# Kernel tuning notes

Measured on AMD Instinct MI355X. Metric: run time of the kernel, lower is better.

## Reference

```python
import jax, jax.numpy as jnp
import numpy as np

N, E = 50000, 800000
H_IN, H, L = 256, 128, 3
EPS = 1e-5  # BatchNorm1d default eps


def setup_inputs() -> dict:
    key = jax.random.key(0)
    ks = jax.random.split(key, 8)
    x = jax.random.normal(ks[0], (N, H_IN), jnp.float32)
    edge_index = jax.random.randint(ks[1], (2, E), 0, N, dtype=jnp.int32)

    def glorot(k, fi, fo):
        lim = np.sqrt(6.0 / (fi + fo)).astype(np.float32)
        return jax.random.uniform(k, (fi, fo), jnp.float32, -lim, lim)

    W_feat = glorot(ks[2], H_IN, H)
    b_feat = jnp.zeros((H,), jnp.float32)
    wkeys = jax.random.split(ks[3], L)
    Ws = jnp.stack([glorot(wkeys[i], H, H) for i in range(L)])
    bs = jnp.zeros((L, H), jnp.float32)
    # BN init per reset_parameters: weight=1, bias=1e-4
    bn_feat_g = jnp.ones((H_IN,), jnp.float32)
    bn_feat_b = jnp.full((H_IN,), 1e-4, jnp.float32)
    bn_g = jnp.ones((L, H), jnp.float32)
    bn_b = jnp.full((L, H), 1e-4, jnp.float32)
    return dict(x=x, edge_index=edge_index, bn_feat_g=bn_feat_g, bn_feat_b=bn_feat_b,
                W_feat=W_feat, b_feat=b_feat, bn_g=bn_g, bn_b=bn_b, Ws=Ws, bs=bs)


def _bn(x, gamma, beta):
    # training-mode BatchNorm1d: batch statistics over nodes, biased variance
    mu = x.mean(0)
    var = x.var(0)
    return (x - mu) * jax.lax.rsqrt(var + EPS) * gamma + beta


def _gcn_norm(edge_index, n):
    # add self-loops (fill value 1) + symmetric deg^-1/2 normalization
    row, col = edge_index[0], edge_index[1]
    loop = jnp.arange(n, dtype=row.dtype)
    row = jnp.concatenate([row, loop])
    col = jnp.concatenate([col, loop])
    deg = jax.ops.segment_sum(jnp.ones_like(row, jnp.float32), row, num_segments=n)
    dinv = jnp.where(deg > 0, jax.lax.rsqrt(deg), 0.0)
    return row, col, dinv[row] * dinv[col]


def _gcn(x, W, b, row, col, norm, n):
    x = x @ W                                   # [n, out]
    msg = x[row] * norm[:, None]                # gather + scale, [E+n, out]
    out = jax.ops.segment_sum(msg, col, num_segments=n)  # scatter-add
    return out + b


def reference(x, edge_index, bn_feat_g, bn_feat_b, W_feat, b_feat, bn_g, bn_b, Ws, bs):
    n = x.shape[0]
    row, col, norm = _gcn_norm(edge_index, n)   # same for every layer
    x = _bn(x, bn_feat_g, bn_feat_b)
    x = _gcn(x, W_feat, b_feat, row, col, norm, n)
    for i in range(L):
        x = _bn(x, bn_g[i], bn_b[i])
        x = _gcn(x, Ws[i], bs[i], row, col, norm, n)
    return x
```

## Files before the change

kernel.cpp:

```cpp
#include <hip/hip_runtime.h>
#include <hip/hip_bf16.h>

#define H_IN 256
#define H    128
#define BN_EPS 1e-5f
#define NCOPY 32
#define NSLICE 256
#define SMAX 5120

using u16 = unsigned short;
using u32 = unsigned int;
typedef __attribute__((ext_vector_type(8))) unsigned short us8;
typedef __attribute__((ext_vector_type(8))) short bf16x8;
typedef __attribute__((ext_vector_type(4))) float f32x4;

__device__ __forceinline__ float b2f(u16 u) {
    return __uint_as_float(((u32)u) << 16);
}
__device__ __forceinline__ u16 f2b(float f) {
    u32 u = __float_as_uint(f);
    u += 0x7FFF + ((u >> 16) & 1);
    return (u16)(u >> 16);
}

__global__ __launch_bounds__(256) void radix1_k(const int* __restrict__ row,
                                                const int* __restrict__ col,
                                                u32* __restrict__ hist_part,
                                                u32* __restrict__ bcnt_part,
                                                int E, int halfN, int hwords) {
    extern __shared__ u32 lds[];
    u32* hist = lds;
    u32* bcnt = lds + hwords;
    int tid = threadIdx.x;
    int slice = blockIdx.x >> 1;
    int half = blockIdx.x & 1;
    for (int i = tid; i < hwords; i += 256) hist[i] = 0;
    bcnt[tid] = 0;
    __syncthreads();

    int len = (E + NSLICE - 1) / NSLICE;
    int e0 = slice * len;
    int e1 = min(e0 + len, E);
    int lo = half * halfN;
    for (int e = e0 + tid; e < e1; e += 256) {
        int r = row[e] - lo;
        if ((u32)r < (u32)halfN)
            atomicAdd(&hist[r >> 1], 1u << ((r & 1) << 4));
        if (half == 0) atomicAdd(&bcnt[((u32)col[e]) >> 8], 1u);
    }
    __syncthreads();
    u32* hdst = hist_part + (size_t)blockIdx.x * hwords;
    for (int i = tid; i < hwords; i += 256) hdst[i] = hist[i];
    if (half == 0) bcnt_part[slice * 256 + tid] = bcnt[tid];
}

__global__ __launch_bounds__(256) void scanb_a_k(const u32* __restrict__ bcnt_part,
                                                 u32* __restrict__ boff,
                                                 u32* __restrict__ btot) {
    __shared__ u32 sh[256];
    int k = blockIdx.x;
    int t = threadIdx.x;
    u32 v = bcnt_part[t * 256 + k];
    sh[t] = v;
    __syncthreads();
    for (int o = 1; o < 256; o <<= 1) {
        u32 x = (t >= o) ? sh[t - o] : 0;
        __syncthreads();
        sh[t] += x;
        __syncthreads();
    }
    boff[t * 256 + k] = sh[t] - v;
    if (t == 255) btot[k] = sh[255];
}

__global__ void scanb_b_k(const u32* __restrict__ btot, u32* __restrict__ bbase) {
    __shared__ u32 sh[256];
    int k = threadIdx.x;
    u32 v = btot[k];
    sh[k] = v;
    __syncthreads();
    for (int o = 1; o < 256; o <<= 1) {
        u32 x = (k >= o) ? sh[k - o] : 0;
        __syncthreads();
        sh[k] += x;
        __syncthreads();
    }
    bbase[k] = sh[k] - v;
    if (k == 255) bbase[256] = sh[255];
}

__global__ void dinv2_k(const u32* __restrict__ hist_part, float* __restrict__ dinv,
                        int N, int halfN, int hwords) {
    int w = blockIdx.x * blockDim.x + threadIdx.x;
    if (w >= 2 * hwords) return;
    int h = (w >= hwords) ? 1 : 0;
    int lw = w - h * hwords;
    u32 v = 0;
    for (int s = 0; s < NSLICE; ++s) v += hist_part[(size_t)(s * 2 + h) * hwords + lw];
    int n = h * halfN + 2 * lw;
    if (n < N)     dinv[n]     = rsqrtf((float)(v & 0xFFFF) + 1.0f);
    if (n + 1 < N) dinv[n + 1] = rsqrtf((float)(v >> 16) + 1.0f);
}

__global__ __launch_bounds__(256) void scat2_k(const int* __restrict__ row,
                                               const int* __restrict__ col,
                                               const u32* __restrict__ boff,
                                               const u32* __restrict__ bbase,
                                               u32* __restrict__ ebuf, int E) {
    __shared__ u32 cur[256];
    int tid = threadIdx.x;
    int slice = blockIdx.x;
    cur[tid] = boff[slice * 256 + tid] + bbase[tid];
    __syncthreads();
    int len = (E + NSLICE - 1) / NSLICE;
    int e0 = slice * len;
    int e1 = min(e0 + len, E);
    for (int e = e0 + tid; e < e1; e += 256) {
        u32 r = (u32)row[e];
        u32 c = (u32)col[e];
        u32 pos = atomicAdd(&cur[c >> 8], 1u);
        ebuf[pos] = r | ((c & 255u) << 16);
    }
}

__global__ __launch_bounds__(256) void sortb_k(const u32* __restrict__ ebuf,
                                               const u32* __restrict__ bbase,
                                               int* __restrict__ rowptr,
                                               u16* __restrict__ esrc, int N) {
    __shared__ u32 est[SMAX];
    __shared__ u32 hist[256], scanv[256], cur[256];
    int b = blockIdx.x, tid = threadIdx.x;
    u32 base = bbase[b];
    int size = (int)(bbase[b + 1] - base);
    int st = min(size, SMAX);
    hist[tid] = 0;
    __syncthreads();
    for (int i = tid; i < st; i += 256) {
        u32 e = ebuf[base + i];
        est[i] = e;
        atomicAdd(&hist[(e >> 16) & 255u], 1u);
    }
    for (int i = SMAX + tid; i < size; i += 256) {
        u32 e = ebuf[base + i];
        atomicAdd(&hist[(e >> 16) & 255u], 1u);
    }
    __syncthreads();
    u32 own = hist[tid];
    scanv[tid] = own;
    __syncthreads();
    for (int o = 1; o < 256; o <<= 1) {
        u32 t = (tid >= o) ? scanv[tid - o] : 0;
        __syncthreads();
        scanv[tid] += t;
        __syncthreads();
    }
    u32 excl = scanv[tid] - own;
    int idx = (b << 8) + tid;
    if (idx <= N) rowptr[idx] = (int)(base + excl);
    cur[tid] = excl;
    __syncthreads();
    for (int i = tid; i < st; i += 256) {
        u32 e = est[i];
        u32 pos = atomicAdd(&cur[(e >> 16) & 255u], 1u);
        esrc[base + pos] = (u16)(e & 0xFFFFu);
    }
    for (int i = SMAX + tid; i < size; i += 256) {
        u32 e = ebuf[base + i];
        u32 pos = atomicAdd(&cur[(e >> 16) & 255u], 1u);
        esrc[base + pos] = (u16)(e & 0xFFFFu);
    }
}

__global__ __launch_bounds__(256) void stats0_k(const float* __restrict__ A,
                                                u16* __restrict__ xb,
                                                float* __restrict__ stats_mc,
                                                int total4, int K) {
    __shared__ float sh[2 * H_IN];
    int tid = threadIdx.x;
    int csz = 2 * K;
    sh[tid] = 0.f;
    sh[tid + 256] = 0.f;
    __syncthreads();
    int gid = blockIdx.x * 256 + tid;
    int stride = gridDim.x * 256;
    int c0 = (gid * 4) % K;
    float s0=0.f,s1=0.f,s2=0.f,s3=0.f, q0=0.f,q1=0.f,q2=0.f,q3=0.f;
    const float4* A4 = (const float4*)A;
    ushort4* X4 = (ushort4*)xb;
    for (int i = gid; i < total4; i += stride) {
        float4 v = A4[i];
        ushort4 xv;
        xv.x = f2b(v.x); xv.y = f2b(v.y); xv.z = f2b(v.z); xv.w = f2b(v.w);
        X4[i] = xv;
        s0 += v.x; q0 += v.x * v.x;
        s1 += v.y; q1 += v.y * v.y;
        s2 += v.z; q2 += v.z * v.z;
        s3 += v.w; q3 += v.w * v.w;
    }
    atomicAdd(&sh[c0],     s0); atomicAdd(&sh[K + c0],     q0);
    atomicAdd(&sh[c0 + 1], s1); atomicAdd(&sh[K + c0 + 1], q1);
    atomicAdd(&sh[c0 + 2], s2); atomicAdd(&sh[K + c0 + 2], q2);
    atomicAdd(&sh[c0 + 3], s3); atomicAdd(&sh[K + c0 + 3], q3);
    __syncthreads();
    float* dst = stats_mc + (size_t)(blockIdx.x & (NCOPY - 1)) * csz;
    for (int i = tid; i < csz; i += 256) atomicAdd(&dst[i], sh[i]);
}

__global__ void fold_k(const float* __restrict__ W, const float* __restrict__ stats_mc,
                       const float* __restrict__ g, const float* __restrict__ b,
                       const float* __restrict__ bias, u16* __restrict__ Wpb,
                       float* __restrict__ bp, int N, int K) {
    int j = blockIdx.x;
    int k = threadIdx.x;
    int csz = 2 * K;
    float sum = 0.f, sumsq = 0.f;
#pragma unroll
    for (int c = 0; c < NCOPY; ++c) {
        sum   += stats_mc[(size_t)c * csz + k];
        sumsq += stats_mc[(size_t)c * csz + K + k];
    }
    float mu = sum / (float)N;
    float var = sumsq / (float)N - mu * mu;
    float s = g[k] * rsqrtf(var + BN_EPS);
    float t = b[k] - mu * s;
    float w = W[(size_t)k * H + j];
    Wpb[(size_t)k * H + j] = f2b(s * w);
    __shared__ float red[256];
    red[k] = t * w;
    __syncthreads();
    for (int o = blockDim.x >> 1; o > 0; o >>= 1) {
        if (k < o) red[k] += red[k + o];
        __syncthreads();
    }
    if (k == 0) bp[j] = bias[j] + red[0];
}

template<int KT>
__global__ __launch_bounds__(256) void gemm_mfma_k(const u16* __restrict__ Ab,
                                                   const u16* __restrict__ Bb,
                                                   u16* __restrict__ Yb, int M) {
    const int K = KT * 32;
    int tid = threadIdx.x;
    int w = tid >> 6;
    int lane = tid & 63;
    int m16 = lane & 15;
    int q = lane >> 4;

    bf16x8 bfrag[KT][2];
#pragma unroll
    for (int t = 0; t < KT; ++t)
#pragma unroll
        for (int p = 0; p < 2; ++p) {
            int ncol = 32 * w + 16 * p + m16;
#pragma unroll
            for (int j = 0; j < 8; ++j)
                bfrag[t][p][j] = (short)Bb[(size_t)(32 * t + 8 * q + j) * H + ncol];
        }

    int nchunk = M >> 4;
    for (int c = blockIdx.x; c < nchunk; c += gridDim.x) {
        int m0 = c << 4;
        const u16* Arow = Ab + (size_t)(m0 + m16) * K + 8 * q;
        bf16x8 afrag[KT];
#pragma unroll
        for (int t = 0; t < KT; ++t)
            afrag[t] = *(const bf16x8*)(Arow + 32 * t);
        f32x4 acc0 = {0.f, 0.f, 0.f, 0.f}, acc1 = {0.f, 0.f, 0.f, 0.f};
#pragma unroll
        for (int t = 0; t < KT; ++t) {
            acc0 = __builtin_amdgcn_mfma_f32_16x16x32_bf16(afrag[t], bfrag[t][0], acc0, 0, 0, 0);
            acc1 = __builtin_amdgcn_mfma_f32_16x16x32_bf16(afrag[t], bfrag[t][1], acc1, 0, 0, 0);
        }
        u16* Crow = Yb + (size_t)(m0 + q * 4) * H + 32 * w + m16;
#pragma unroll
        for (int i = 0; i < 4; ++i) {
            Crow[(size_t)i * H]      = f2b(acc0[i]);
            Crow[(size_t)i * H + 16] = f2b(acc1[i]);
        }
    }
}

__global__ __launch_bounds__(256) void csragg_k(const int* __restrict__ rowptr,
                                                const u16* __restrict__ esrc,
                                                const u16* __restrict__ Yb,
                                                const float* __restrict__ dinv,
                                                const float* __restrict__ bp,
                                                u16* __restrict__ Ob,
                                                float* __restrict__ Of,
                                                float* __restrict__ stats_mc,
                                                int do_stats, int N) {
    __shared__ float sh[1024];
    int tid = threadIdx.x;
    int node = blockIdx.x * 16 + (tid >> 4);
    int fl = tid & 15;
    float o[8] = {0.f,0.f,0.f,0.f,0.f,0.f,0.f,0.f};
    if (node < N) {
        const us8* Y8 = (const us8*)Yb;
        float dn = dinv[node];
        float acc[8];
        {
            us8 ys = Y8[(size_t)node * 16 + fl];
#pragma unroll
            for (int j = 0; j < 8; ++j) acc[j] = dn * b2f(ys[j]);
        }
        int s = rowptr[node], e = rowptr[node + 1];
        int p = s;
        for (; p + 1 < e; p += 2) {
            int s0 = esrc[p], s1 = esrc[p + 1];
            float n0 = dinv[s0], n1 = dinv[s1];
            us8 v0 = Y8[(size_t)s0 * 16 + fl];
            us8 v1 = Y8[(size_t)s1 * 16 + fl];
#pragma unroll
            for (int j = 0; j < 8; ++j) acc[j] += n0 * b2f(v0[j]);
#pragma unroll
            for (int j = 0; j < 8; ++j) acc[j] += n1 * b2f(v1[j]);
        }
        if (p < e) {
            int s0 = esrc[p];
            float n0 = dinv[s0];
            us8 v0 = Y8[(size_t)s0 * 16 + fl];
#pragma unroll
            for (int j = 0; j < 8; ++j) acc[j] += n0 * b2f(v0[j]);
        }
        float4 b0 = ((const float4*)bp)[fl * 2];
        float4 b1 = ((const float4*)bp)[fl * 2 + 1];
        o[0] = b0.x + dn * acc[0]; o[1] = b0.y + dn * acc[1];
        o[2] = b0.z + dn * acc[2]; o[3] = b0.w + dn * acc[3];
        o[4] = b1.x + dn * acc[4]; o[5] = b1.y + dn * acc[5];
        o[6] = b1.z + dn * acc[6]; o[7] = b1.w + dn * acc[7];
        if (Of) {
            float4* O4 = (float4*)Of;
            O4[(size_t)node * 32 + fl * 2]     = make_float4(o[0], o[1], o[2], o[3]);
            O4[(size_t)node * 32 + fl * 2 + 1] = make_float4(o[4], o[5], o[6], o[7]);
        } else {
            us8 ov;
#pragma unroll
            for (int j = 0; j < 8; ++j) ov[j] = f2b(o[j]);
            *(us8*)(Ob + (size_t)node * H + fl * 8) = ov;
        }
    }
    if (do_stats) {
        float sv[16];
#pragma unroll
        for (int j = 0; j < 8; ++j) { sv[j] = o[j]; sv[8 + j] = o[j] * o[j]; }
#pragma unroll
        for (int j = 0; j < 16; ++j) {
            sv[j] += __shfl_xor(sv[j], 16, 64);
            sv[j] += __shfl_xor(sv[j], 32, 64);
        }
        int lane = tid & 63, wv = tid >> 6;
        if (lane < 16) {
            float* base = sh + wv * 256;
#pragma unroll
            for (int j = 0; j < 8; ++j) {
                base[fl * 8 + j]       = sv[j];
                base[128 + fl * 8 + j] = sv[8 + j];
            }
        }
        __syncthreads();
        float v = sh[tid] + sh[256 + tid] + sh[512 + tid] + sh[768 + tid];
        atomicAdd(&stats_mc[(size_t)(blockIdx.x & (NCOPY - 1)) * (2 * H) + tid], v);
    }
}

extern "C" void kernel_launch(void* const* d_in, const int* in_sizes, int n_in,
                              void* d_out, int out_size, void* d_ws, size_t ws_size,
                              hipStream_t stream) {
    const float* x     = (const float*)d_in[0];
    const int*   ei    = (const int*)d_in[1];
    const float* bnfg  = (const float*)d_in[2];
    const float* bnfb  = (const float*)d_in[3];
    const float* Wfeat = (const float*)d_in[4];
    const float* bfeat = (const float*)d_in[5];
    const float* bng   = (const float*)d_in[6];
    const float* bnb   = (const float*)d_in[7];
    const float* Ws    = (const float*)d_in[8];
    const float* bs    = (const float*)d_in[9];

    int N = in_sizes[0] / H_IN;
    int E = in_sizes[1] / 2;
    const int* row = ei;
    const int* col = ei + E;

    int halfN  = (N + 1) / 2;
    int hwords = (halfN + 1) / 2;
    int NB     = (N + 255) >> 8;

    char* p = (char*)d_ws;
    auto alloc = [&](size_t bytes) { char* r = p; p += (bytes + 63) & ~size_t(63); return r; };
    float* dinv      = (float*)alloc(N * 4);
    float* stats_mc  = (float*)alloc(NCOPY * 2 * H_IN * 4);
    u16*   Wpb       = (u16*)alloc(H_IN * H * 2);
    float* bp        = (float*)alloc(H * 4);
    u32*   hist_part = (u32*)alloc((size_t)NSLICE * 2 * hwords * 4);
    u32*   bcnt_part = (u32*)alloc(NSLICE * 256 * 4);
    u32*   boff      = (u32*)alloc(NSLICE * 256 * 4);
    u32*   btot      = (u32*)alloc(256 * 4);
    u32*   bbase     = (u32*)alloc(260 * 4);
    int*   rowptr    = (int*)alloc((N + 1) * 4);
    u32*   ebuf      = (u32*)alloc((size_t)E * 4);
    u16*   esrc      = (u16*)alloc((size_t)E * 2);
    u16*   xb        = (u16*)alloc((size_t)N * H_IN * 2);
    u16*   Yb        = (u16*)alloc((size_t)N * H * 2);
    u16*   ACTb      = (u16*)alloc((size_t)N * H * 2);

    float* out = (float*)d_out;

    size_t r1_lds = (size_t)(hwords + 256) * 4;
    radix1_k<<<2 * NSLICE, 256, r1_lds, stream>>>(row, col, hist_part, bcnt_part, E, halfN, hwords);
    scanb_a_k<<<256, 256, 0, stream>>>(bcnt_part, boff, btot);
    scanb_b_k<<<1, 256, 0, stream>>>(btot, bbase);
    dinv2_k<<<(2 * hwords + 255) / 256, 256, 0, stream>>>(hist_part, dinv, N, halfN, hwords);
    scat2_k<<<NSLICE, 256, 0, stream>>>(row, col, boff, bbase, ebuf, E);
    sortb_k<<<NB, 256, 0, stream>>>(ebuf, bbase, rowptr, esrc, N);

    hipMemsetAsync(stats_mc, 0, NCOPY * 2 * H_IN * sizeof(float), stream);
    stats0_k<<<512, 256, 0, stream>>>(x, xb, stats_mc, N * H_IN / 4, H_IN);

    for (int l = 0; l < 4; ++l) {
        const u16* Ab     = (l == 0) ? xb : ACTb;
        int K             = (l == 0) ? H_IN : H;
        const float* W    = (l == 0) ? Wfeat : Ws + (size_t)(l - 1) * H * H;
        const float* bias = (l == 0) ? bfeat : bs + (size_t)(l - 1) * H;
        const float* g    = (l == 0) ? bnfg : bng + (size_t)(l - 1) * H;
        const float* bb   = (l == 0) ? bnfb : bnb + (size_t)(l - 1) * H;
        int do_stats      = (l < 3);

        fold_k<<<H, K, 0, stream>>>(W, stats_mc, g, bb, bias, Wpb, bp, N, K);
        if (l == 0) gemm_mfma_k<8><<<512, 256, 0, stream>>>(Ab, Wpb, Yb, N);
        else        gemm_mfma_k<4><<<512, 256, 0, stream>>>(Ab, Wpb, Yb, N);
        if (do_stats)
            hipMemsetAsync(stats_mc, 0, NCOPY * 2 * H * sizeof(float), stream);
        csragg_k<<<(N + 15) / 16, 256, 0, stream>>>(rowptr, esrc, Yb, dinv, bp,
                                                    ACTb, (l == 3) ? out : nullptr,
                                                    stats_mc, do_stats, N);
    }
}
```

Measured before the change: 397.3 us.

## Merge setup kernels, fold stats zeroing into kernels, transpose weights, unroll gather

```diff
diff --git a/kernel.cpp b/kernel.cpp
--- a/kernel.cpp
+++ b/kernel.cpp
@@ -7,6 +7,7 @@
 #define NCOPY 32
 #define NSLICE 256
 #define SMAX 5120
+#define STATS_FLOATS (NCOPY * 2 * H_IN)
 
 using u16 = unsigned short;
 using u32 = unsigned int;
@@ -54,23 +55,43 @@
     if (half == 0) bcnt_part[slice * 256 + tid] = bcnt[tid];
 }
 
-__global__ __launch_bounds__(256) void scanb_a_k(const u32* __restrict__ bcnt_part,
-                                                 u32* __restrict__ boff,
-                                                 u32* __restrict__ btot) {
-    __shared__ u32 sh[256];
-    int k = blockIdx.x;
-    int t = threadIdx.x;
-    u32 v = bcnt_part[t * 256 + k];
-    sh[t] = v;
-    __syncthreads();
-    for (int o = 1; o < 256; o <<= 1) {
-        u32 x = (t >= o) ? sh[t - o] : 0;
-        __syncthreads();
-        sh[t] += x;
-        __syncthreads();
-    }
-    boff[t * 256 + k] = sh[t] - v;
-    if (t == 255) btot[k] = sh[255];
+#define ZB 64
+__global__ __launch_bounds__(256) void mid_k(const u32* __restrict__ bcnt_part,
+                                             u32* __restrict__ boff,
+                                             u32* __restrict__ btot,
+                                             const u32* __restrict__ hist_part,
+                                             float* __restrict__ dinv,
+                                             float* __restrict__ stats_mc,
+                                             int N, int halfN, int hwords) {
+    int b = blockIdx.x;
+    int tid = threadIdx.x;
+    if (b < 256) {
+        __shared__ u32 sh[256];
+        u32 v = bcnt_part[tid * 256 + b];
+        sh[tid] = v;
+        __syncthreads();
+        for (int o = 1; o < 256; o <<= 1) {
+            u32 x = (tid >= o) ? sh[tid - o] : 0;
+            __syncthreads();
+            sh[tid] += x;
+            __syncthreads();
+        }
+        boff[tid * 256 + b] = sh[tid] - v;
+        if (tid == 255) btot[b] = sh[255];
+    } else if (b < 256 + ZB) {
+        int i = (b - 256) * 256 + tid;
+        if (i < STATS_FLOATS) stats_mc[i] = 0.f;
+    } else {
+        int w = (b - 256 - ZB) * 256 + tid;
+        if (w >= 2 * hwords) return;
+        int h = (w >= hwords) ? 1 : 0;
+        int lw = w - h * hwords;
+        u32 v = 0;
+        for (int s = 0; s < NSLICE; ++s) v += hist_part[(size_t)(s * 2 + h) * hwords + lw];
+        int n = h * halfN + 2 * lw;
+        if (n < N)     dinv[n]     = rsqrtf((float)(v & 0xFFFF) + 1.0f);
+        if (n + 1 < N) dinv[n + 1] = rsqrtf((float)(v >> 16) + 1.0f);
+    }
 }
 
 __global__ void scanb_b_k(const u32* __restrict__ btot, u32* __restrict__ bbase) {
@@ -87,19 +108,6 @@
     }
     bbase[k] = sh[k] - v;
     if (k == 255) bbase[256] = sh[255];
-}
-
-__global__ void dinv2_k(const u32* __restrict__ hist_part, float* __restrict__ dinv,
-                        int N, int halfN, int hwords) {
-    int w = blockIdx.x * blockDim.x + threadIdx.x;
-    if (w >= 2 * hwords) return;
-    int h = (w >= hwords) ? 1 : 0;
-    int lw = w - h * hwords;
-    u32 v = 0;
-    for (int s = 0; s < NSLICE; ++s) v += hist_part[(size_t)(s * 2 + h) * hwords + lw];
-    int n = h * halfN + 2 * lw;
-    if (n < N)     dinv[n]     = rsqrtf((float)(v & 0xFFFF) + 1.0f);
-    if (n + 1 < N) dinv[n + 1] = rsqrtf((float)(v >> 16) + 1.0f);
 }
 
 __global__ __launch_bounds__(256) void scat2_k(const int* __restrict__ row,
@@ -208,7 +216,7 @@
 
 __global__ void fold_k(const float* __restrict__ W, const float* __restrict__ stats_mc,
                        const float* __restrict__ g, const float* __restrict__ b,
-                       const float* __restrict__ bias, u16* __restrict__ Wpb,
+                       const float* __restrict__ bias, u16* __restrict__ Wt,
                        float* __restrict__ bp, int N, int K) {
     int j = blockIdx.x;
     int k = threadIdx.x;
@@ -224,7 +232,7 @@
     float s = g[k] * rsqrtf(var + BN_EPS);
     float t = b[k] - mu * s;
     float w = W[(size_t)k * H + j];
-    Wpb[(size_t)k * H + j] = f2b(s * w);
+    Wt[(size_t)j * K + k] = f2b(s * w);
     __shared__ float red[256];
     red[k] = t * w;
     __syncthreads();
@@ -237,10 +245,14 @@
 
 template<int KT>
 __global__ __launch_bounds__(256) void gemm_mfma_k(const u16* __restrict__ Ab,
-                                                   const u16* __restrict__ Bb,
-                                                   u16* __restrict__ Yb, int M) {
+                                                   const u16* __restrict__ Wt,
+                                                   u16* __restrict__ Yb, int M,
+                                                   float* __restrict__ stats_z) {
     const int K = KT * 32;
     int tid = threadIdx.x;
+    if (stats_z && blockIdx.x == 0) {
+        for (int i = tid; i < STATS_FLOATS; i += 256) stats_z[i] = 0.f;
+    }
     int w = tid >> 6;
     int lane = tid & 63;
     int m16 = lane & 15;
@@ -252,9 +264,7 @@
 #pragma unroll
         for (int p = 0; p < 2; ++p) {
             int ncol = 32 * w + 16 * p + m16;
-#pragma unroll
-            for (int j = 0; j < 8; ++j)
-                bfrag[t][p][j] = (short)Bb[(size_t)(32 * t + 8 * q + j) * H + ncol];
+            bfrag[t][p] = *(const bf16x8*)(Wt + (size_t)ncol * K + 32 * t + 8 * q);
         }
 
     int nchunk = M >> 4;
@@ -305,17 +315,23 @@
         }
         int s = rowptr[node], e = rowptr[node + 1];
         int p = s;
-        for (; p + 1 < e; p += 2) {
-            int s0 = esrc[p], s1 = esrc[p + 1];
-            float n0 = dinv[s0], n1 = dinv[s1];
+        for (; p + 3 < e; p += 4) {
+            int s0 = esrc[p], s1 = esrc[p + 1], s2 = esrc[p + 2], s3 = esrc[p + 3];
+            float n0 = dinv[s0], n1 = dinv[s1], n2 = dinv[s2], n3 = dinv[s3];
             us8 v0 = Y8[(size_t)s0 * 16 + fl];
             us8 v1 = Y8[(size_t)s1 * 16 + fl];
+            us8 v2 = Y8[(size_t)s2 * 16 + fl];
+            us8 v3 = Y8[(size_t)s3 * 16 + fl];
 #pragma unroll
             for (int j = 0; j < 8; ++j) acc[j] += n0 * b2f(v0[j]);
 #pragma unroll
             for (int j = 0; j < 8; ++j) acc[j] += n1 * b2f(v1[j]);
-        }
-        if (p < e) {
+#pragma unroll
+            for (int j = 0; j < 8; ++j) acc[j] += n2 * b2f(v2[j]);
+#pragma unroll
+            for (int j = 0; j < 8; ++j) acc[j] += n3 * b2f(v3[j]);
+        }
+        for (; p < e; ++p) {
             int s0 = esrc[p];
             float n0 = dinv[s0];
             us8 v0 = Y8[(size_t)s0 * 16 + fl];
@@ -389,8 +405,8 @@
     char* p = (char*)d_ws;
     auto alloc = [&](size_t bytes) { char* r = p; p += (bytes + 63) & ~size_t(63); return r; };
     float* dinv      = (float*)alloc(N * 4);
-    float* stats_mc  = (float*)alloc(NCOPY * 2 * H_IN * 4);
-    u16*   Wpb       = (u16*)alloc(H_IN * H * 2);
+    float* stats_mc  = (float*)alloc(STATS_FLOATS * 4);
+    u16*   Wt        = (u16*)alloc(H_IN * H * 2);
     float* bp        = (float*)alloc(H * 4);
     u32*   hist_part = (u32*)alloc((size_t)NSLICE * 2 * hwords * 4);
     u32*   bcnt_part = (u32*)alloc(NSLICE * 256 * 4);
@@ -408,13 +424,13 @@
 
     size_t r1_lds = (size_t)(hwords + 256) * 4;
     radix1_k<<<2 * NSLICE, 256, r1_lds, stream>>>(row, col, hist_part, bcnt_part, E, halfN, hwords);
-    scanb_a_k<<<256, 256, 0, stream>>>(bcnt_part, boff, btot);
+    int dblocks = (2 * hwords + 255) / 256;
+    mid_k<<<256 + ZB + dblocks, 256, 0, stream>>>(bcnt_part, boff, btot, hist_part,
+                                                  dinv, stats_mc, N, halfN, hwords);
     scanb_b_k<<<1, 256, 0, stream>>>(btot, bbase);
-    dinv2_k<<<(2 * hwords + 255) / 256, 256, 0, stream>>>(hist_part, dinv, N, halfN, hwords);
     scat2_k<<<NSLICE, 256, 0, stream>>>(row, col, boff, bbase, ebuf, E);
     sortb_k<<<NB, 256, 0, stream>>>(ebuf, bbase, rowptr, esrc, N);
 
-    hipMemsetAsync(stats_mc, 0, NCOPY * 2 * H_IN * sizeof(float), stream);
     stats0_k<<<512, 256, 0, stream>>>(x, xb, stats_mc, N * H_IN / 4, H_IN);
 
     for (int l = 0; l < 4; ++l) {
@@ -426,11 +442,10 @@
         const float* bb   = (l == 0) ? bnfb : bnb + (size_t)(l - 1) * H;
         int do_stats      = (l < 3);
 
-        fold_k<<<H, K, 0, stream>>>(W, stats_mc, g, bb, bias, Wpb, bp, N, K);
-        if (l == 0) gemm_mfma_k<8><<<512, 256, 0, stream>>>(Ab, Wpb, Yb, N);
-        else        gemm_mfma_k<4><<<512, 256, 0, stream>>>(Ab, Wpb, Yb, N);
-        if (do_stats)
-            hipMemsetAsync(stats_mc, 0, NCOPY * 2 * H * sizeof(float), stream);
+        fold_k<<<H, K, 0, stream>>>(W, stats_mc, g, bb, bias, Wt, bp, N, K);
+        float* sz = do_stats ? stats_mc : nullptr;
+        if (l == 0) gemm_mfma_k<8><<<512, 256, 0, stream>>>(Ab, Wt, Yb, N, sz);
+        else        gemm_mfma_k<4><<<512, 256, 0, stream>>>(Ab, Wt, Yb, N, sz);
         csragg_k<<<(N + 15) / 16, 256, 0, stream>>>(rowptr, esrc, Yb, dinv, bp,
                                                     ACTb, (l == 3) ? out : nullptr,
                                                     stats_mc, do_stats, N);
```

After: 378.8 us. 4.7% less time.
